# Kernel optimization log

Measured on AMD Instinct MI355X. Metric: run time of the kernel, lower is better.

The kernel has to match this reference:

```python
import jax, jax.numpy as jnp
import numpy as np

BS = 8192
INPUT_DIM = 4096
LAYER_DIMS = [64, 256, 64]
BLOCK_DIM = LAYER_DIMS[0]
N_BLOCKS = INPUT_DIM // BLOCK_DIM


def setup_inputs() -> dict:
    key = jax.random.key(0)
    kx, kw1, kw2 = jax.random.split(key, 3)
    x = jax.random.normal(kx, (BS, INPUT_DIM), dtype=jnp.float32)
    # BlockLinear params: weight ~ randn, bias ~ zeros (as in torch source)
    W1 = jax.random.normal(kw1, (N_BLOCKS, LAYER_DIMS[0], LAYER_DIMS[1]), dtype=jnp.float32)
    b1 = jnp.zeros((N_BLOCKS, 1, LAYER_DIMS[1]), dtype=jnp.float32)
    W2 = jax.random.normal(kw2, (N_BLOCKS, LAYER_DIMS[1], LAYER_DIMS[2]), dtype=jnp.float32)
    b2 = jnp.zeros((N_BLOCKS, 1, LAYER_DIMS[2]), dtype=jnp.float32)
    return {"x": x, "W1": W1, "b1": b1, "W2": W2, "b2": b2}


def reference(x, W1, b1, W2, b2):
    bs = x.shape[0]
    # [bs, input_dim] -> [n_blocks, bs, block_dim]
    h = x.reshape(bs, N_BLOCKS, BLOCK_DIM).transpose(1, 0, 2)
    # BlockLinear 1 (bmm + bias) then exact GELU (torch nn.GELU default)
    h = jnp.einsum('nbi,nio->nbo', h, W1) + b1
    h = jax.nn.gelu(h, approximate=False)
    # BlockLinear 2
    h = jnp.einsum('nbi,nio->nbo', h, W2) + b2
    # [n_blocks, bs, out_block] -> [bs, n_blocks*out_block]
    return h.transpose(1, 0, 2).reshape(bs, -1)
```

## Files before the change

### kernel.cpp

```cpp
#include <hip/hip_runtime.h>

using f16x8 = _Float16 __attribute__((ext_vector_type(8)));
using f32x4 = float __attribute__((ext_vector_type(4)));

#define BS      8192
#define IN_DIM  4096
#define NB      64
#define BD      64
#define HID     256
#define OD      64
#define GYP     8
#define SLABS   4

__device__ __forceinline__ float gelu_f(float z) {
    float e = __builtin_amdgcn_exp2f(z * -2.4554443f);
    float r = __builtin_amdgcn_rcpf(e + 1.0f);
    return z * r;
}

__global__ __launch_bounds__(256) void prep_weights(
    const float* __restrict__ w1g, const float* __restrict__ w2g,
    f16x8* __restrict__ ws1, f16x8* __restrict__ ws2) {
    const int n = blockIdx.x;
    const int t = threadIdx.x;
    const float* W1n = w1g + (size_t)n * (BD * HID);
    const float* W2n = w2g + (size_t)n * (HID * OD);
    #pragma unroll
    for (int it = 0; it < 8; ++it) {
        int e = it * 256 + t;
        {
            int ht = e >> 7, ks = (e >> 6) & 1, le = e & 63;
            int ge = le >> 4, oo = le & 15;
            f16x8 v;
            #pragma unroll
            for (int j = 0; j < 8; ++j)
                v[j] = (_Float16)W1n[(size_t)(ks * 32 + ge * 8 + j) * HID + ht * 16 + oo];
            ws1[(size_t)n * 2048 + e] = v;
        }
        {
            int p = e >> 8, n2 = (e >> 6) & 3, le = e & 63;
            int ge = le >> 4, ce = le & 15;
            f16x8 v;
            #pragma unroll
            for (int j = 0; j < 8; ++j)
                v[j] = (_Float16)W2n[(size_t)(p * 32 + ((j >> 2) << 4) + ge * 4 + (j & 3)) * OD + n2 * 16 + ce];
            ws2[(size_t)n * 2048 + e] = v;
        }
    }
}

__global__ __launch_bounds__(512, 4) void blockmlp_kernel(
    const float* __restrict__ xg,
    const f16x8* __restrict__ ws1, const f16x8* __restrict__ ws2,
    const float* __restrict__ b1g, const float* __restrict__ b2g,
    float* __restrict__ outg) {

    __shared__ f16x8 W1F[2048];
    __shared__ f16x8 W2L[2048];
    __shared__ float b1L[HID];

    const int tid = threadIdx.x;
    const int w   = tid >> 6;
    const int l   = tid & 63;
    const int g   = l >> 4;
    const int l15 = l & 15;
    const int n   = blockIdx.x;

    const f16x8* p1 = ws1 + (size_t)n * 2048;
    const f16x8* p2 = ws2 + (size_t)n * 2048;
    f16x8 s1[4], s2[4];
    #pragma unroll
    for (int it = 0; it < 4; ++it) { s1[it] = p1[it * 512 + tid]; }
    #pragma unroll
    for (int it = 0; it < 4; ++it) { s2[it] = p2[it * 512 + tid]; }
    #pragma unroll
    for (int it = 0; it < 4; ++it) { W1F[it * 512 + tid] = s1[it]; }
    #pragma unroll
    for (int it = 0; it < 4; ++it) { W2L[it * 512 + tid] = s2[it]; }

    if (tid < HID) b1L[tid] = b1g[n * HID + tid];

    float b2b[4];
    #pragma unroll
    for (int n2 = 0; n2 < 4; ++n2) b2b[n2] = b2g[n * OD + n2 * 16 + l15];

    __syncthreads();

    const int base = blockIdx.y * (SLABS * 256) + w * 32;

    #pragma unroll
    for (int s = 0; s < SLABS; ++s) {
        const int row0 = base + s * 256;

        f16x8 xa[2][2];
        #pragma unroll
        for (int rs = 0; rs < 2; ++rs)
            #pragma unroll
            for (int ks = 0; ks < 2; ++ks) {
                const float* px = xg + (size_t)(row0 + rs * 16 + l15) * IN_DIM + n * BD + ks * 32 + g * 8;
                float4 lo = *(const float4*)px;
                float4 hi = *(const float4*)(px + 4);
                f16x8 v;
                v[0] = (_Float16)lo.x; v[1] = (_Float16)lo.y;
                v[2] = (_Float16)lo.z; v[3] = (_Float16)lo.w;
                v[4] = (_Float16)hi.x; v[5] = (_Float16)hi.y;
                v[6] = (_Float16)hi.z; v[7] = (_Float16)hi.w;
                xa[rs][ks] = v;
            }

        f32x4 c2[2][4];
        #pragma unroll
        for (int rs = 0; rs < 2; ++rs)
            #pragma unroll
            for (int n2 = 0; n2 < 4; ++n2) {
                f32x4 ci;
                ci[0] = b2b[n2]; ci[1] = b2b[n2]; ci[2] = b2b[n2]; ci[3] = b2b[n2];
                c2[rs][n2] = ci;
            }

        #pragma unroll
        for (int p = 0; p < 8; ++p) {
            f32x4 c1[2][2];
            #pragma unroll
            for (int htl = 0; htl < 2; ++htl) {
                f32x4 ca = *(const f32x4*)&b1L[(p * 2 + htl) * 16 + g * 4];
                f32x4 cb = ca;
                #pragma unroll
                for (int ks = 0; ks < 2; ++ks) {
                    f16x8 wf = W1F[(((p * 2 + htl) * 2) + ks) * 64 + l];
                    ca = __builtin_amdgcn_mfma_f32_16x16x32_f16(wf, xa[0][ks], ca, 0, 0, 0);
                    cb = __builtin_amdgcn_mfma_f32_16x16x32_f16(wf, xa[1][ks], cb, 0, 0, 0);
                }
                c1[htl][0] = ca; c1[htl][1] = cb;
            }
            f16x8 a2[2];
            #pragma unroll
            for (int rs = 0; rs < 2; ++rs) {
                f16x8 v;
                #pragma unroll
                for (int q = 0; q < 4; ++q) {
                    v[q]     = (_Float16)gelu_f(c1[0][rs][q]);
                    v[q + 4] = (_Float16)gelu_f(c1[1][rs][q]);
                }
                a2[rs] = v;
            }
            #pragma unroll
            for (int n2 = 0; n2 < 4; ++n2) {
                f16x8 bf = W2L[(p * 4 + n2) * 64 + l];
                c2[0][n2] = __builtin_amdgcn_mfma_f32_16x16x32_f16(a2[0], bf, c2[0][n2], 0, 0, 0);
                c2[1][n2] = __builtin_amdgcn_mfma_f32_16x16x32_f16(a2[1], bf, c2[1][n2], 0, 0, 0);
            }
        }

        #pragma unroll
        for (int rs = 0; rs < 2; ++rs)
            #pragma unroll
            for (int n2 = 0; n2 < 4; ++n2)
                #pragma unroll
                for (int q = 0; q < 4; ++q) {
                    int row = row0 + rs * 16 + g * 4 + q;
                    outg[(size_t)row * IN_DIM + n * BD + n2 * 16 + l15] = c2[rs][n2][q];
                }
    }
}

extern "C" void kernel_launch(void* const* d_in, const int* in_sizes, int n_in,
                              void* d_out, int out_size, void* d_ws, size_t ws_size,
                              hipStream_t stream) {
    const float* x  = (const float*)d_in[0];
    const float* W1 = (const float*)d_in[1];
    const float* b1 = (const float*)d_in[2];
    const float* W2 = (const float*)d_in[3];
    const float* b2 = (const float*)d_in[4];
    float* out = (float*)d_out;

    f16x8* ws1 = (f16x8*)d_ws;
    f16x8* ws2 = ws1 + (size_t)NB * 2048;

    hipLaunchKernelGGL(prep_weights, dim3(NB), dim3(256), 0, stream, W1, W2, ws1, ws2);
    hipLaunchKernelGGL(blockmlp_kernel, dim3(NB, GYP), dim3(512), 0, stream,
                       x, ws1, ws2, b1, b2, out);
}
```

Before: 78.90 us.

## Process 64 rows per wave in one pass instead of four 32-row slabs

Each wave now handles 64 rows (4 row-subtiles) at once instead of looping over 4 slabs of 32 rows, and the grid doubles in y to cover the batch. Each LDS weight fragment is reused across 4 MFMAs rather than 2, which halves LDS weight reads per row, and each block still does its own weight staging. The cost is more accumulator registers, so the launch bounds drop to 2 blocks per SM, which lowers occupancy and removes the slab loop that overlapped x loads with compute.

```diff
diff --git a/kernel.cpp b/kernel.cpp
--- a/kernel.cpp
+++ b/kernel.cpp
@@ -9,8 +9,8 @@
 #define BD      64
 #define HID     256
 #define OD      64
-#define GYP     8
-#define SLABS   4
+#define GYP     16
+#define RS      4
 
 __device__ __forceinline__ float gelu_f(float z) {
     float e = __builtin_amdgcn_exp2f(z * -2.4554443f);
@@ -49,7 +49,7 @@
     }
 }
 
-__global__ __launch_bounds__(512, 4) void blockmlp_kernel(
+__global__ __launch_bounds__(512, 2) void blockmlp_kernel(
     const float* __restrict__ xg,
     const f16x8* __restrict__ ws1, const f16x8* __restrict__ ws2,
     const float* __restrict__ b1g, const float* __restrict__ b2g,
@@ -86,82 +86,79 @@
 
     __syncthreads();
 
-    const int base = blockIdx.y * (SLABS * 256) + w * 32;
+    const int row0 = blockIdx.y * 512 + w * 64;
+
+    f16x8 xa[RS][2];
+    #pragma unroll
+    for (int rs = 0; rs < RS; ++rs)
+        #pragma unroll
+        for (int ks = 0; ks < 2; ++ks) {
+            const float* px = xg + (size_t)(row0 + rs * 16 + l15) * IN_DIM + n * BD + ks * 32 + g * 8;
+            float4 lo = *(const float4*)px;
+            float4 hi = *(const float4*)(px + 4);
+            f16x8 v;
+            v[0] = (_Float16)lo.x; v[1] = (_Float16)lo.y;
+            v[2] = (_Float16)lo.z; v[3] = (_Float16)lo.w;
+            v[4] = (_Float16)hi.x; v[5] = (_Float16)hi.y;
+            v[6] = (_Float16)hi.z; v[7] = (_Float16)hi.w;
+            xa[rs][ks] = v;
+        }
+
+    f32x4 c2[RS][4];
+    #pragma unroll
+    for (int rs = 0; rs < RS; ++rs)
+        #pragma unroll
+        for (int n2 = 0; n2 < 4; ++n2) {
+            f32x4 ci;
+            ci[0] = b2b[n2]; ci[1] = b2b[n2]; ci[2] = b2b[n2]; ci[3] = b2b[n2];
+            c2[rs][n2] = ci;
+        }
 
     #pragma unroll
-    for (int s = 0; s < SLABS; ++s) {
-        const int row0 = base + s * 256;
-
-        f16x8 xa[2][2];
+    for (int p = 0; p < 8; ++p) {
+        f32x4 c1[2][RS];
         #pragma unroll
-        for (int rs = 0; rs < 2; ++rs)
+        for (int htl = 0; htl < 2; ++htl) {
+            f32x4 cb = *(const f32x4*)&b1L[(p * 2 + htl) * 16 + g * 4];
+            #pragma unroll
+            for (int rs = 0; rs < RS; ++rs) c1[htl][rs] = cb;
             #pragma unroll
             for (int ks = 0; ks < 2; ++ks) {
-                const float* px = xg + (size_t)(row0 + rs * 16 + l15) * IN_DIM + n * BD + ks * 32 + g * 8;
-                float4 lo = *(const float4*)px;
-                float4 hi = *(const float4*)(px + 4);
-                f16x8 v;
-                v[0] = (_Float16)lo.x; v[1] = (_Float16)lo.y;
-                v[2] = (_Float16)lo.z; v[3] = (_Float16)lo.w;
-                v[4] = (_Float16)hi.x; v[5] = (_Float16)hi.y;
-                v[6] = (_Float16)hi.z; v[7] = (_Float16)hi.w;
-                xa[rs][ks] = v;
-            }
-
-        f32x4 c2[2][4];
-        #pragma unroll
-        for (int rs = 0; rs < 2; ++rs)
-            #pragma unroll
-            for (int n2 = 0; n2 < 4; ++n2) {
-                f32x4 ci;
-                ci[0] = b2b[n2]; ci[1] = b2b[n2]; ci[2] = b2b[n2]; ci[3] = b2b[n2];
-                c2[rs][n2] = ci;
-            }
-
-        #pragma unroll
-        for (int p = 0; p < 8; ++p) {
-            f32x4 c1[2][2];
-            #pragma unroll
-            for (int htl = 0; htl < 2; ++htl) {
-                f32x4 ca = *(const f32x4*)&b1L[(p * 2 + htl) * 16 + g * 4];
-                f32x4 cb = ca;
+                f16x8 wf = W1F[(((p * 2 + htl) * 2) + ks) * 64 + l];
                 #pragma unroll
-                for (int ks = 0; ks < 2; ++ks) {
-                    f16x8 wf = W1F[(((p * 2 + htl) * 2) + ks) * 64 + l];
-                    ca = __builtin_amdgcn_mfma_f32_16x16x32_f16(wf, xa[0][ks], ca, 0, 0, 0);
-                    cb = __builtin_amdgcn_mfma_f32_16x16x32_f16(wf, xa[1][ks], cb, 0, 0, 0);
-                }
-                c1[htl][0] = ca; c1[htl][1] = cb;
-            }
-            f16x8 a2[2];
-            #pragma unroll
-            for (int rs = 0; rs < 2; ++rs) {
-                f16x8 v;
-                #pragma unroll
-                for (int q = 0; q < 4; ++q) {
-                    v[q]     = (_Float16)gelu_f(c1[0][rs][q]);
-                    v[q + 4] = (_Float16)gelu_f(c1[1][rs][q]);
-                }
-                a2[rs] = v;
-            }
-            #pragma unroll
-            for (int n2 = 0; n2 < 4; ++n2) {
-                f16x8 bf = W2L[(p * 4 + n2) * 64 + l];
-                c2[0][n2] = __builtin_amdgcn_mfma_f32_16x16x32_f16(a2[0], bf, c2[0][n2], 0, 0, 0);
-                c2[1][n2] = __builtin_amdgcn_mfma_f32_16x16x32_f16(a2[1], bf, c2[1][n2], 0, 0, 0);
+                for (int rs = 0; rs < RS; ++rs)
+                    c1[htl][rs] = __builtin_amdgcn_mfma_f32_16x16x32_f16(wf, xa[rs][ks], c1[htl][rs], 0, 0, 0);
             }
         }
+        f16x8 a2[RS];
+        #pragma unroll
+        for (int rs = 0; rs < RS; ++rs) {
+            f16x8 v;
+            #pragma unroll
+            for (int q = 0; q < 4; ++q) {
+                v[q]     = (_Float16)gelu_f(c1[0][rs][q]);
+                v[q + 4] = (_Float16)gelu_f(c1[1][rs][q]);
+            }
+            a2[rs] = v;
+        }
+        #pragma unroll
+        for (int n2 = 0; n2 < 4; ++n2) {
+            f16x8 bf = W2L[(p * 4 + n2) * 64 + l];
+            #pragma unroll
+            for (int rs = 0; rs < RS; ++rs)
+                c2[rs][n2] = __builtin_amdgcn_mfma_f32_16x16x32_f16(a2[rs], bf, c2[rs][n2], 0, 0, 0);
+        }
+    }
 
+    #pragma unroll
+    for (int rs = 0; rs < RS; ++rs)
         #pragma unroll
-        for (int rs = 0; rs < 2; ++rs)
+        for (int n2 = 0; n2 < 4; ++n2)
             #pragma unroll
-            for (int n2 = 0; n2 < 4; ++n2)
-                #pragma unroll
-                for (int q = 0; q < 4; ++q) {
-                    int row = row0 + rs * 16 + g * 4 + q;
-                    outg[(size_t)row * IN_DIM + n * BD + n2 * 16 + l15] = c2[rs][n2][q];
-                }
-    }
+            for (int q = 0; q < 4; ++q) {
+                int row = row0 + rs * 16 + g * 4 + q;
+                outg[(size_t)row * IN_DIM + n * BD + n2 * 16 + l15] = c2[rs][n2][q];
+            }
 }
 
 extern "C" void kernel_launch(void* const* d_in, const int* in_sizes, int n_in,
```

Measured after the change: 78.61 us. About the same (-0.4%).

## Software-pipeline two row-subtiles so GELU overlaps MFMA, stagger wave start

Applied to the files above, without the earlier changes.

Splits the two 16-row subtiles into separate A/B streams and interleaves them, so the first GEMM of one subtile (and of the next hidden chunk) is issued while the other subtile's GELU and second GEMM run. This aims to hide the latency of the transcendental GELU work behind matrix-core work within a wave. It also adds a per-wave s_sleep stagger after the barrier so the eight waves do not all hit global memory and the matrix cores in lockstep. The stagger adds a small fixed delay, and the interleaving may raise register pressure under the 512x4 launch bounds.

```diff
diff --git a/kernel.cpp b/kernel.cpp
--- a/kernel.cpp
+++ b/kernel.cpp
@@ -86,7 +86,38 @@
 
     __syncthreads();
 
+    for (int i = 0; i < w; ++i) __builtin_amdgcn_s_sleep(4);
+
     const int base = blockIdx.y * (SLABS * 256) + w * 32;
+
+    auto gemm1 = [&](int p, f32x4 (&c1)[2], const f16x8 (&xv)[2]) {
+        #pragma unroll
+        for (int htl = 0; htl < 2; ++htl) {
+            f32x4 c = *(const f32x4*)&b1L[(p * 2 + htl) * 16 + g * 4];
+            #pragma unroll
+            for (int ks = 0; ks < 2; ++ks) {
+                f16x8 wf = W1F[(((p * 2 + htl) * 2) + ks) * 64 + l];
+                c = __builtin_amdgcn_mfma_f32_16x16x32_f16(wf, xv[ks], c, 0, 0, 0);
+            }
+            c1[htl] = c;
+        }
+    };
+    auto gelu8 = [&](const f32x4 (&c1)[2]) {
+        f16x8 v;
+        #pragma unroll
+        for (int q = 0; q < 4; ++q) {
+            v[q]     = (_Float16)gelu_f(c1[0][q]);
+            v[q + 4] = (_Float16)gelu_f(c1[1][q]);
+        }
+        return v;
+    };
+    auto gemm2 = [&](int p, f16x8 a2v, f32x4 (&cacc)[4]) {
+        #pragma unroll
+        for (int n2 = 0; n2 < 4; ++n2) {
+            f16x8 bf = W2L[(p * 4 + n2) * 64 + l];
+            cacc[n2] = __builtin_amdgcn_mfma_f32_16x16x32_f16(a2v, bf, cacc[n2], 0, 0, 0);
+        }
+    };
 
     #pragma unroll
     for (int s = 0; s < SLABS; ++s) {
@@ -108,59 +139,35 @@
                 xa[rs][ks] = v;
             }
 
-        f32x4 c2[2][4];
+        f32x4 c2A[4], c2B[4];
         #pragma unroll
-        for (int rs = 0; rs < 2; ++rs)
-            #pragma unroll
-            for (int n2 = 0; n2 < 4; ++n2) {
-                f32x4 ci;
-                ci[0] = b2b[n2]; ci[1] = b2b[n2]; ci[2] = b2b[n2]; ci[3] = b2b[n2];
-                c2[rs][n2] = ci;
-            }
+        for (int n2 = 0; n2 < 4; ++n2) {
+            f32x4 ci;
+            ci[0] = b2b[n2]; ci[1] = b2b[n2]; ci[2] = b2b[n2]; ci[3] = b2b[n2];
+            c2A[n2] = ci; c2B[n2] = ci;
+        }
 
+        f32x4 c1A[2], c1B[2];
+        gemm1(0, c1A, xa[0]);
         #pragma unroll
         for (int p = 0; p < 8; ++p) {
-            f32x4 c1[2][2];
-            #pragma unroll
-            for (int htl = 0; htl < 2; ++htl) {
-                f32x4 ca = *(const f32x4*)&b1L[(p * 2 + htl) * 16 + g * 4];
-                f32x4 cb = ca;
-                #pragma unroll
-                for (int ks = 0; ks < 2; ++ks) {
-                    f16x8 wf = W1F[(((p * 2 + htl) * 2) + ks) * 64 + l];
-                    ca = __builtin_amdgcn_mfma_f32_16x16x32_f16(wf, xa[0][ks], ca, 0, 0, 0);
-                    cb = __builtin_amdgcn_mfma_f32_16x16x32_f16(wf, xa[1][ks], cb, 0, 0, 0);
-                }
-                c1[htl][0] = ca; c1[htl][1] = cb;
-            }
-            f16x8 a2[2];
-            #pragma unroll
-            for (int rs = 0; rs < 2; ++rs) {
-                f16x8 v;
-                #pragma unroll
-                for (int q = 0; q < 4; ++q) {
-                    v[q]     = (_Float16)gelu_f(c1[0][rs][q]);
-                    v[q + 4] = (_Float16)gelu_f(c1[1][rs][q]);
-                }
-                a2[rs] = v;
-            }
-            #pragma unroll
-            for (int n2 = 0; n2 < 4; ++n2) {
-                f16x8 bf = W2L[(p * 4 + n2) * 64 + l];
-                c2[0][n2] = __builtin_amdgcn_mfma_f32_16x16x32_f16(a2[0], bf, c2[0][n2], 0, 0, 0);
-                c2[1][n2] = __builtin_amdgcn_mfma_f32_16x16x32_f16(a2[1], bf, c2[1][n2], 0, 0, 0);
-            }
+            gemm1(p, c1B, xa[1]);
+            f16x8 a2A = gelu8(c1A);
+            gemm2(p, a2A, c2A);
+            if (p < 7) gemm1(p + 1, c1A, xa[0]);
+            f16x8 a2B = gelu8(c1B);
+            gemm2(p, a2B, c2B);
         }
 
         #pragma unroll
-        for (int rs = 0; rs < 2; ++rs)
+        for (int n2 = 0; n2 < 4; ++n2)
             #pragma unroll
-            for (int n2 = 0; n2 < 4; ++n2)
-                #pragma unroll
-                for (int q = 0; q < 4; ++q) {
-                    int row = row0 + rs * 16 + g * 4 + q;
-                    outg[(size_t)row * IN_DIM + n * BD + n2 * 16 + l15] = c2[rs][n2][q];
-                }
+            for (int q = 0; q < 4; ++q) {
+                int rowA = row0 + g * 4 + q;
+                outg[(size_t)rowA * IN_DIM + n * BD + n2 * 16 + l15] = c2A[n2][q];
+                int rowB = row0 + 16 + g * 4 + q;
+                outg[(size_t)rowB * IN_DIM + n * BD + n2 * 16 + l15] = c2B[n2][q];
+            }
     }
 }
 
```

Measured after the change: 115.9 us. 1.47x slower.

## Double-buffer x tiles in LDS via async global_load_lds with swizzle

Applied to the files above, without the earlier changes.

Input rows are now staged into a double-buffered LDS tile using async global-to-LDS loads with an XOR swizzle, prefetching the next 128-row slab while the current one is computed. Each wave handles 16 rows per slab instead of 32, and the grid shrinks to 4 row groups with 16 slabs each. The aim is to hide global load latency behind MFMA work. In exchange it adds 64KB of LDS, which lowers occupancy, a block-wide barrier per slab, and half the MFMA work per wave per slab.

```diff
diff --git a/kernel.cpp b/kernel.cpp
--- a/kernel.cpp
+++ b/kernel.cpp
@@ -9,8 +9,9 @@
 #define BD      64
 #define HID     256
 #define OD      64
-#define GYP     8
-#define SLABS   4
+#define GYP     4
+#define SLABS   16
+#define SROWS   128
 
 __device__ __forceinline__ float gelu_f(float z) {
     float e = __builtin_amdgcn_exp2f(z * -2.4554443f);
@@ -58,6 +59,7 @@
     __shared__ f16x8 W1F[2048];
     __shared__ f16x8 W2L[2048];
     __shared__ float b1L[HID];
+    __shared__ float xbuf[2][SROWS * 64];
 
     const int tid = threadIdx.x;
     const int w   = tid >> 6;
@@ -84,83 +86,102 @@
     #pragma unroll
     for (int n2 = 0; n2 < 4; ++n2) b2b[n2] = b2g[n * OD + n2 * 16 + l15];
 
+    const int wgrow = blockIdx.y * (SLABS * SROWS);
+
+    #pragma unroll
+    for (int i = 0; i < 4; ++i) {
+        int e = i * 512 + tid;
+        int r = e >> 4, c = e & 15;
+        int cs = c ^ (r & 7);
+        const float* src = xg + (size_t)(wgrow + r) * IN_DIM + n * BD + cs * 4;
+        __builtin_amdgcn_global_load_lds(
+            (const __attribute__((address_space(1))) void*)src,
+            (__attribute__((address_space(3))) void*)&xbuf[0][(i * 512 + (tid & 448)) * 4],
+            16, 0, 0);
+    }
+
     __syncthreads();
 
-    const int base = blockIdx.y * (SLABS * 256) + w * 32;
-
-    #pragma unroll
     for (int s = 0; s < SLABS; ++s) {
-        const int row0 = base + s * 256;
-
-        f16x8 xa[2][2];
+        const int cur = s & 1;
+        const int row0 = wgrow + s * SROWS;
+
+        if (s + 1 < SLABS) {
+            #pragma unroll
+            for (int i = 0; i < 4; ++i) {
+                int e = i * 512 + tid;
+                int r = e >> 4, c = e & 15;
+                int cs = c ^ (r & 7);
+                const float* src = xg + (size_t)(row0 + SROWS + r) * IN_DIM + n * BD + cs * 4;
+                __builtin_amdgcn_global_load_lds(
+                    (const __attribute__((address_space(1))) void*)src,
+                    (__attribute__((address_space(3))) void*)&xbuf[cur ^ 1][(i * 512 + (tid & 448)) * 4],
+                    16, 0, 0);
+            }
+        }
+
+        f16x8 xa[2];
+        {
+            const int r = w * 16 + l15;
+            const float* xb = &xbuf[cur][r * 64];
+            #pragma unroll
+            for (int ks = 0; ks < 2; ++ks) {
+                int pc0 = (ks * 8 + g * 2 + 0) ^ (l15 & 7);
+                int pc1 = (ks * 8 + g * 2 + 1) ^ (l15 & 7);
+                f32x4 c0 = *(const f32x4*)&xb[pc0 * 4];
+                f32x4 c1v = *(const f32x4*)&xb[pc1 * 4];
+                f16x8 v;
+                v[0] = (_Float16)c0[0]; v[1] = (_Float16)c0[1];
+                v[2] = (_Float16)c0[2]; v[3] = (_Float16)c0[3];
+                v[4] = (_Float16)c1v[0]; v[5] = (_Float16)c1v[1];
+                v[6] = (_Float16)c1v[2]; v[7] = (_Float16)c1v[3];
+                xa[ks] = v;
+            }
+        }
+
+        f32x4 c2[4];
         #pragma unroll
-        for (int rs = 0; rs < 2; ++rs)
-            #pragma unroll
-            for (int ks = 0; ks < 2; ++ks) {
-                const float* px = xg + (size_t)(row0 + rs * 16 + l15) * IN_DIM + n * BD + ks * 32 + g * 8;
-                float4 lo = *(const float4*)px;
-                float4 hi = *(const float4*)(px + 4);
-                f16x8 v;
-                v[0] = (_Float16)lo.x; v[1] = (_Float16)lo.y;
-                v[2] = (_Float16)lo.z; v[3] = (_Float16)lo.w;
-                v[4] = (_Float16)hi.x; v[5] = (_Float16)hi.y;
-                v[6] = (_Float16)hi.z; v[7] = (_Float16)hi.w;
-                xa[rs][ks] = v;
-            }
-
-        f32x4 c2[2][4];
-        #pragma unroll
-        for (int rs = 0; rs < 2; ++rs)
-            #pragma unroll
-            for (int n2 = 0; n2 < 4; ++n2) {
-                f32x4 ci;
-                ci[0] = b2b[n2]; ci[1] = b2b[n2]; ci[2] = b2b[n2]; ci[3] = b2b[n2];
-                c2[rs][n2] = ci;
-            }
+        for (int n2 = 0; n2 < 4; ++n2) {
+            f32x4 ci;
+            ci[0] = b2b[n2]; ci[1] = b2b[n2]; ci[2] = b2b[n2]; ci[3] = b2b[n2];
+            c2[n2] = ci;
+        }
 
         #pragma unroll
         for (int p = 0; p < 8; ++p) {
-            f32x4 c1[2][2];
+            f32x4 c1[2];
             #pragma unroll
             for (int htl = 0; htl < 2; ++htl) {
-                f32x4 ca = *(const f32x4*)&b1L[(p * 2 + htl) * 16 + g * 4];
-                f32x4 cb = ca;
+                f32x4 c = *(const f32x4*)&b1L[(p * 2 + htl) * 16 + g * 4];
                 #pragma unroll
                 for (int ks = 0; ks < 2; ++ks) {
                     f16x8 wf = W1F[(((p * 2 + htl) * 2) + ks) * 64 + l];
-                    ca = __builtin_amdgcn_mfma_f32_16x16x32_f16(wf, xa[0][ks], ca, 0, 0, 0);
-                    cb = __builtin_amdgcn_mfma_f32_16x16x32_f16(wf, xa[1][ks], cb, 0, 0, 0);
+                    c = __builtin_amdgcn_mfma_f32_16x16x32_f16(wf, xa[ks], c, 0, 0, 0);
                 }
-                c1[htl][0] = ca; c1[htl][1] = cb;
-            }
-            f16x8 a2[2];
-            #pragma unroll
-            for (int rs = 0; rs < 2; ++rs) {
-                f16x8 v;
-                #pragma unroll
-                for (int q = 0; q < 4; ++q) {
-                    v[q]     = (_Float16)gelu_f(c1[0][rs][q]);
-                    v[q + 4] = (_Float16)gelu_f(c1[1][rs][q]);
-                }
-                a2[rs] = v;
+                c1[htl] = c;
+            }
+            f16x8 a2;
+            #pragma unroll
+            for (int q = 0; q < 4; ++q) {
+                a2[q]     = (_Float16)gelu_f(c1[0][q]);
+                a2[q + 4] = (_Float16)gelu_f(c1[1][q]);
             }
             #pragma unroll
             for (int n2 = 0; n2 < 4; ++n2) {
                 f16x8 bf = W2L[(p * 4 + n2) * 64 + l];
-                c2[0][n2] = __builtin_amdgcn_mfma_f32_16x16x32_f16(a2[0], bf, c2[0][n2], 0, 0, 0);
-                c2[1][n2] = __builtin_amdgcn_mfma_f32_16x16x32_f16(a2[1], bf, c2[1][n2], 0, 0, 0);
+                c2[n2] = __builtin_amdgcn_mfma_f32_16x16x32_f16(a2, bf, c2[n2], 0, 0, 0);
             }
         }
 
         #pragma unroll
-        for (int rs = 0; rs < 2; ++rs)
-            #pragma unroll
-            for (int n2 = 0; n2 < 4; ++n2)
-                #pragma unroll
-                for (int q = 0; q < 4; ++q) {
-                    int row = row0 + rs * 16 + g * 4 + q;
-                    outg[(size_t)row * IN_DIM + n * BD + n2 * 16 + l15] = c2[rs][n2][q];
-                }
+        for (int n2 = 0; n2 < 4; ++n2)
+            #pragma unroll
+            for (int q = 0; q < 4; ++q) {
+                int row = row0 + w * 16 + g * 4 + q;
+                outg[(size_t)row * IN_DIM + n * BD + n2 * 16 + l15] = c2[n2][q];
+            }
+
+        __syncthreads();
     }
 }
 
```

Result: slower. 88.16 us (+11.7%).
